# Kernel optimization log

Hardware: AMD Instinct MI355X
Metric: run time of the kernel (lower is better)

The kernel has to match this reference:

```python
import jax, jax.numpy as jnp
import numpy as np

HIDDEN = 1024
N_HEAD = 16
HEAD_DIM = HIDDEN // N_HEAD


def setup_inputs() -> dict:
    key = jax.random.key(0)
    k1, k2, k3 = jax.random.split(key, 3)
    B, S = 4, 2048
    x = jax.random.normal(k1, (B, S, HIDDEN), dtype=jnp.float32)
    # nn.Linear(hidden, 3*hidden, bias=False): weight [3*hidden, hidden]
    w_qkv = jax.random.normal(k2, (3 * HIDDEN, HIDDEN), dtype=jnp.float32) * (HIDDEN ** -0.5)
    w_out = jax.random.normal(k3, (HIDDEN, HIDDEN), dtype=jnp.float32) * (HIDDEN ** -0.5)
    return {"x": x, "w_qkv": w_qkv, "w_out": w_out}


def _rope(q, k):
    # q, k: [B, H, S, D]
    S, D = q.shape[-2], q.shape[-1]
    pos = jnp.arange(S, dtype=jnp.float32)[:, None]          # [S, 1]
    ids = jnp.arange(D // 2, dtype=jnp.float32)              # [D/2]
    theta = jnp.power(jnp.float32(10000.0), 2.0 * ids / D)   # [D/2]
    ang = pos / theta                                        # [S, D/2]
    # torch code: sin at even slots, cos at odd slots; then repeat_interleave(2)
    sin = jnp.repeat(jnp.sin(ang), 2, axis=-1)               # [S, D]
    cos = jnp.repeat(jnp.cos(ang), 2, axis=-1)               # [S, D]

    def rot(t):
        # stack([-t_odd, t_even], -1).reshape -> interleaved rotate-half
        t2 = jnp.stack([-t[..., 1::2], t[..., 0::2]], axis=-1).reshape(t.shape)
        return t * cos + t2 * sin

    return rot(q), rot(k)


def reference(x, w_qkv, w_out):
    B, S, _ = x.shape
    qkv = jnp.einsum('bsd,ed->bse', x, w_qkv)                # [B, S, 3*hidden]
    qkv = qkv.reshape(B, S, N_HEAD, 3 * HEAD_DIM).transpose(0, 2, 1, 3)  # [B,H,S,3D]
    q, k, v = jnp.split(qkv, 3, axis=-1)                     # each [B,H,S,D]
    q, k = _rope(q, k)
    # NOTE: original forward never applies self.scale, mask (eval), or dropout.
    scores = jnp.einsum('bhqd,bhkd->bhqk', q, k)             # [B,H,S,S]
    probs = jax.nn.softmax(scores, axis=-1)
    out = jnp.einsum('bhqk,bhkd->bhqd', probs, v)            # [B,H,S,D]
    out = out.transpose(0, 2, 1, 3).reshape(B, S, HIDDEN)
    return jnp.einsum('bsd,ed->bse', out, w_out)
```

## Files before the change

kernel.cpp:

```cpp
#include <hip/hip_runtime.h>
#include <stdint.h>
#include <math.h>

#define NHEAD 16
#define HDIM 64
#define BATCH 4
#define SEQ 2048
#define NROWS (BATCH*SEQ)
#define LOG2E 1.4426950408889634f

typedef _Float16 f16x8 __attribute__((ext_vector_type(8)));
typedef _Float16 f16x4 __attribute__((ext_vector_type(4)));
typedef __fp16 h16x2 __attribute__((ext_vector_type(2)));
typedef float f32x4 __attribute__((ext_vector_type(4)));
typedef float f32x16 __attribute__((ext_vector_type(16)));
typedef unsigned int u32x4 __attribute__((ext_vector_type(4)));

typedef const __attribute__((address_space(1))) unsigned int* gas_ptr;
typedef __attribute__((address_space(3))) unsigned int* las_ptr;

__device__ __forceinline__ void gload_lds16(const void* g, void* l) {
  __builtin_amdgcn_global_load_lds((gas_ptr)g, (las_ptr)l, 16, 0, 0);
}

__device__ __forceinline__ float exp2_fast(float x) {
  float r; asm("v_exp_f32 %0, %1" : "=v"(r) : "v"(x)); return r;
}

__device__ __forceinline__ unsigned pku(float a, float b) {
  h16x2 p = __builtin_amdgcn_cvt_pkrtz(a, b);
  return __builtin_bit_cast(unsigned, p);
}

__global__ void cvt_f16_kernel(const float* __restrict__ in,
                               unsigned short* __restrict__ out, int n4) {
  int stride = gridDim.x * blockDim.x;
  for (int i = blockIdx.x * blockDim.x + threadIdx.x; i < n4; i += stride) {
    float4 v = ((const float4*)in)[i];
    f16x4 h;
    h[0] = (_Float16)v.x; h[1] = (_Float16)v.y;
    h[2] = (_Float16)v.z; h[3] = (_Float16)v.w;
    ((f16x4*)out)[i] = h;
  }
}

__global__ void sincos_kernel(float2* __restrict__ tab) {
  int idx = blockIdx.x * blockDim.x + threadIdx.x;
  int s = idx >> 5, i = idx & 31;
  float theta = powf(10000.0f, (float)i / 32.0f);
  float ang = (float)s / theta;
  tab[idx] = make_float2(sinf(ang), cosf(ang));
}

__global__ __launch_bounds__(256)
void gemm_qkv_f16(const unsigned short* __restrict__ A,
                  const unsigned short* __restrict__ B,
                  const float2* __restrict__ tab,
                  unsigned short* __restrict__ Qh,
                  unsigned short* __restrict__ Kh,
                  unsigned short* __restrict__ Vt) {
  const int K = 1024, N = 3072, nk = K >> 5;
  __shared__ unsigned short sA[2][128 * 32];
  __shared__ unsigned short sB[2][128 * 32];
  const int tid = threadIdx.x;
  const int lane = tid & 63;
  const int wave = tid >> 6;
  const int wr = wave >> 1, wc = wave & 1;
  const long m0 = (long)blockIdx.x * 128;
  const long n0 = (long)blockIdx.y * 128;

  f32x4 acc[4][4] = {};

  const int o0 = tid * 16;
  const int row0_ = o0 >> 6;
  const int colb0 = o0 & 63;

  auto stage = [&](int buf, int kt) {
    const long k0 = (long)kt * 32;
    const char* Ab = (const char*)A;
    const char* Bb = (const char*)B;
    gload_lds16(Ab + ((m0 + row0_) * K + k0) * 2 + colb0,      (char*)&sA[buf][0] + o0);
    gload_lds16(Ab + ((m0 + row0_ + 64) * K + k0) * 2 + colb0, (char*)&sA[buf][0] + o0 + 4096);
    gload_lds16(Bb + ((n0 + row0_) * K + k0) * 2 + colb0,      (char*)&sB[buf][0] + o0);
    gload_lds16(Bb + ((n0 + row0_ + 64) * K + k0) * 2 + colb0, (char*)&sB[buf][0] + o0 + 4096);
  };

  stage(0, 0);
  __syncthreads();
  int cur = 0;
  const int kq = (lane >> 4) * 8;
  const int rA = wr * 64 + (lane & 15);
  const int rB = wc * 64 + (lane & 15);

  for (int kt = 0; kt < nk; ++kt) {
    if (kt + 1 < nk) stage(cur ^ 1, kt + 1);
    f16x8 af[4], bfr[4];
#pragma unroll
    for (int m = 0; m < 4; ++m)
      af[m] = *(const f16x8*)&sA[cur][(rA + m * 16) * 32 + kq];
#pragma unroll
    for (int n = 0; n < 4; ++n)
      bfr[n] = *(const f16x8*)&sB[cur][(rB + n * 16) * 32 + kq];
#pragma unroll
    for (int m = 0; m < 4; ++m)
#pragma unroll
      for (int n = 0; n < 4; ++n)
        acc[m][n] = __builtin_amdgcn_mfma_f32_16x16x32_f16(af[m], bfr[n], acc[m][n], 0, 0, 0);
    __syncthreads();
    cur ^= 1;
  }

  const int lhi = lane >> 4, llo = lane & 15;
  const long rbase = m0 + wr * 64 + (lhi << 2);
  const long cbase = n0 + wc * 64 + llo;
#pragma unroll
  for (int m = 0; m < 4; ++m)
#pragma unroll
    for (int n = 0; n < 4; ++n)
#pragma unroll
      for (int r = 0; r < 4; ++r) {
        int row = (int)(rbase + m * 16 + r);
        int col = (int)(cbase + n * 16);
        float v = acc[m][n][r];
        float p = __shfl_xor(v, 1, 64);
        int s = row & 2047, b = row >> 11;
        int h = col / 192, off = col % 192;
        int part = off >> 6, d = off & 63;
        long bh_ = b * 16 + h;
        if (part < 2) {
          float2 sc = tab[s * 32 + (d >> 1)];
          float rot = (d & 1) ? (v * sc.y + p * sc.x) : (v * sc.y - p * sc.x);
          long idx = (bh_ * SEQ + s) * 64 + d;
          if (part == 0) ((_Float16*)Qh)[idx] = (_Float16)(rot * LOG2E);
          else           ((_Float16*)Kh)[idx] = (_Float16)rot;
        } else {
          ((_Float16*)Vt)[(bh_ * 64 + d) * SEQ + s] = (_Float16)v;
        }
      }
}

__global__ __launch_bounds__(512, 3)
void attn_kernel(const unsigned short* __restrict__ Qh,
                 const unsigned short* __restrict__ Kh,
                 const unsigned short* __restrict__ Vt,
                 unsigned short* __restrict__ AOut) {
  __shared__ unsigned short sK[2][64 * 64];
  __shared__ unsigned short sV[2][64 * 64];

  const int tid = threadIdx.x;
  const int w = tid >> 6, lane = tid & 63;
  const int q32 = lane & 31, hi = lane >> 5;
  const int bh = blockIdx.y, b = bh >> 4, h = bh & 15;
  const int q = blockIdx.x * 256 + w * 32 + q32;

  f16x8 aq[4];
#pragma unroll
  for (int ds = 0; ds < 4; ++ds)
    aq[ds] = *(const f16x8*)&Qh[((long)bh * SEQ + q) * 64 + ds * 16 + hi * 8];

  f32x16 acc0 = {}, acc1 = {};
  float mrow = -INFINITY, lrow = 0.f;

  const int r7 = q32 & 7;
  int off[2][4];
#pragma unroll
  for (int t = 0; t < 2; ++t)
#pragma unroll
    for (int s = 0; s < 4; ++s)
      off[t][s] = (t * 32 + q32) * 64 + (((s * 2 + hi) ^ r7) << 3);

  const int cr = tid >> 3, cp = tid & 7, cps = cp ^ (cr & 7);
  const long kSrc0 = ((long)bh * SEQ + cr) * 64 + cps * 8;
  const long vSrc0 = ((long)bh * 64 + cr) * SEQ + cps * 8;

  auto stage = [&](int buf, int kt) {
    gload_lds16(&Kh[kSrc0 + (long)kt * 4096], (char*)&sK[buf][0] + tid * 16);
    gload_lds16(&Vt[vSrc0 + (long)kt * 64],   (char*)&sV[buf][0] + tid * 16);
  };

  stage(0, 0);
  __syncthreads();

#define MKPA(dst, S, R0) {                                        \
    unsigned A0 = pku(S[R0 + 0], S[R0 + 1]);                      \
    unsigned A1 = pku(S[R0 + 2], S[R0 + 3]);                      \
    unsigned B0 = pku(S[R0 + 4], S[R0 + 5]);                      \
    unsigned B1 = pku(S[R0 + 6], S[R0 + 7]);                      \
    asm("v_permlane32_swap_b32 %0, %1" : "+v"(A0), "+v"(B0));     \
    asm("v_permlane32_swap_b32 %0, %1" : "+v"(A1), "+v"(B1));     \
    u32x4 tt; tt[0] = A0; tt[1] = A1; tt[2] = B0; tt[3] = B1;     \
    dst = __builtin_bit_cast(f16x8, tt); }

#pragma unroll 2
  for (int kt = 0; kt < SEQ / 64; ++kt) {
    const int cur = kt & 1;
    if (kt + 1 < SEQ / 64) stage(cur ^ 1, kt + 1);
    const unsigned short* Kb = &sK[cur][0];
    const unsigned short* Vb = &sV[cur][0];

    f32x16 s0v = {}, s1v = {};
    __builtin_amdgcn_s_setprio(1);
#pragma unroll
    for (int ds = 0; ds < 4; ++ds) {
      f16x8 k0 = *(const f16x8*)&Kb[off[0][ds]];
      f16x8 k1 = *(const f16x8*)&Kb[off[1][ds]];
      s0v = __builtin_amdgcn_mfma_f32_32x32x16_f16(k0, aq[ds], s0v, 0, 0, 0);
      s1v = __builtin_amdgcn_mfma_f32_32x32x16_f16(k1, aq[ds], s1v, 0, 0, 0);
    }
    __builtin_amdgcn_s_setprio(0);

    float ta[16];
#pragma unroll
    for (int r = 0; r < 16; ++r) ta[r] = fmaxf(s0v[r], s1v[r]);
#pragma unroll
    for (int d = 8; d > 0; d >>= 1)
#pragma unroll
      for (int r = 0; r < d; ++r) ta[r] = fmaxf(ta[r], ta[r + d]);
    float tmax = fmaxf(ta[0], __shfl_xor(ta[0], 32, 64));

    if (__any(tmax > mrow + 8.0f)) {
      float mnew = fmaxf(mrow, tmax);
      float al = exp2_fast(mrow - mnew);
      mrow = mnew;
#pragma unroll
      for (int r = 0; r < 16; ++r) { acc0[r] *= al; acc1[r] *= al; }
      lrow *= al;
    }
    const float mr = mrow;

#pragma unroll
    for (int r = 0; r < 16; ++r) {
      s0v[r] = exp2_fast(s0v[r] - mr);
      s1v[r] = exp2_fast(s1v[r] - mr);
    }

    float sa[16];
#pragma unroll
    for (int r = 0; r < 16; ++r) sa[r] = s0v[r] + s1v[r];
#pragma unroll
    for (int d = 8; d > 0; d >>= 1)
#pragma unroll
      for (int r = 0; r < d; ++r) sa[r] = sa[r] + sa[r + d];
    lrow += sa[0] + __shfl_xor(sa[0], 32, 64);

    f16x8 pa[4];
    MKPA(pa[0], s0v, 0);
    MKPA(pa[1], s0v, 8);
    MKPA(pa[2], s1v, 0);
    MKPA(pa[3], s1v, 8);

    __builtin_amdgcn_s_setprio(1);
#pragma unroll
    for (int ks = 0; ks < 4; ++ks) {
      f16x8 v0 = *(const f16x8*)&Vb[off[0][ks]];
      f16x8 v1 = *(const f16x8*)&Vb[off[1][ks]];
      acc0 = __builtin_amdgcn_mfma_f32_32x32x16_f16(v0, pa[ks], acc0, 0, 0, 0);
      acc1 = __builtin_amdgcn_mfma_f32_32x32x16_f16(v1, pa[ks], acc1, 0, 0, 0);
    }
    __builtin_amdgcn_s_setprio(0);
    __syncthreads();
  }

  float inv = 1.f / lrow;
  const long obase = ((long)b * SEQ + q) * 1024 + h * 64;
#define EPI(ACCV, DT)                                              \
  {                                                                \
    _Pragma("unroll")                                              \
    for (int rg = 0; rg < 4; ++rg) {                               \
      f16x4 o;                                                     \
      _Pragma("unroll")                                            \
      for (int e = 0; e < 4; ++e)                                  \
        o[e] = (_Float16)(ACCV[rg * 4 + e] * inv);                 \
      *(f16x4*)&AOut[obase + DT * 32 + rg * 8 + hi * 4] = o;       \
    }                                                              \
  }
  EPI(acc0, 0);
  EPI(acc1, 1);
}

__global__ __launch_bounds__(256)
void gemm_out_f16(const unsigned short* __restrict__ A,
                  const unsigned short* __restrict__ B,
                  float* __restrict__ C, int M, int N, int K) {
  __shared__ unsigned short sA[2][128 * 32];
  __shared__ unsigned short sB[2][128 * 32];
  const int tid = threadIdx.x;
  const int lane = tid & 63;
  const int wave = tid >> 6;
  const int wr = wave >> 1, wc = wave & 1;
  const long m0 = (long)blockIdx.x * 128;
  const long n0 = (long)blockIdx.y * 128;

  f32x4 acc[4][4] = {};

  const int o0 = tid * 16;
  const int row0_ = o0 >> 6;
  const int colb0 = o0 & 63;

  auto stage = [&](int buf, int kt) {
    const long k0 = (long)kt * 32;
    const char* Ab = (const char*)A;
    const char* Bb = (const char*)B;
    gload_lds16(Ab + ((m0 + row0_) * K + k0) * 2 + colb0,      (char*)&sA[buf][0] + o0);
    gload_lds16(Ab + ((m0 + row0_ + 64) * K + k0) * 2 + colb0, (char*)&sA[buf][0] + o0 + 4096);
    gload_lds16(Bb + ((n0 + row0_) * K + k0) * 2 + colb0,      (char*)&sB[buf][0] + o0);
    gload_lds16(Bb + ((n0 + row0_ + 64) * K + k0) * 2 + colb0, (char*)&sB[buf][0] + o0 + 4096);
  };

  const int nk = K >> 5;
  stage(0, 0);
  __syncthreads();
  int cur = 0;
  const int kq = (lane >> 4) * 8;
  const int rA = wr * 64 + (lane & 15);
  const int rB = wc * 64 + (lane & 15);

  for (int kt = 0; kt < nk; ++kt) {
    if (kt + 1 < nk) stage(cur ^ 1, kt + 1);
    f16x8 af[4], bfr[4];
#pragma unroll
    for (int m = 0; m < 4; ++m)
      af[m] = *(const f16x8*)&sA[cur][(rA + m * 16) * 32 + kq];
#pragma unroll
    for (int n = 0; n < 4; ++n)
      bfr[n] = *(const f16x8*)&sB[cur][(rB + n * 16) * 32 + kq];
#pragma unroll
    for (int m = 0; m < 4; ++m)
#pragma unroll
      for (int n = 0; n < 4; ++n)
        acc[m][n] = __builtin_amdgcn_mfma_f32_16x16x32_f16(af[m], bfr[n], acc[m][n], 0, 0, 0);
    __syncthreads();
    cur ^= 1;
  }

  const long rbase = m0 + wr * 64 + ((lane >> 4) << 2);
  const long cbase = n0 + wc * 64 + (lane & 15);
#pragma unroll
  for (int m = 0; m < 4; ++m)
#pragma unroll
    for (int n = 0; n < 4; ++n)
#pragma unroll
      for (int r = 0; r < 4; ++r) {
        long row = rbase + m * 16 + r;
        long col = cbase + n * 16;
        C[row * N + col] = acc[m][n][r];
      }
}

extern "C" void kernel_launch(void* const* d_in, const int* in_sizes, int n_in,
                              void* d_out, int out_size, void* d_ws, size_t ws_size,
                              hipStream_t stream) {
  const float* x     = (const float*)d_in[0];
  const float* w_qkv = (const float*)d_in[1];
  const float* w_out = (const float*)d_in[2];
  float* out = (float*)d_out;
  char* ws = (char*)d_ws;

  unsigned short* xb    = (unsigned short*)(ws + 0);
  unsigned short* attnb = xb;
  unsigned short* wqkvb = (unsigned short*)(ws + 16777216);
  unsigned short* woutb = (unsigned short*)(ws + 23068672);
  unsigned short* Qh    = (unsigned short*)(ws + 25165824);
  unsigned short* Kh    = (unsigned short*)(ws + 41943040);
  unsigned short* Vt    = (unsigned short*)(ws + 58720256);
  float2*         tab   = (float2*)(ws + 75497472);

  cvt_f16_kernel<<<2048, 256, 0, stream>>>(x, xb, NROWS * 1024 / 4);
  cvt_f16_kernel<<<1024, 256, 0, stream>>>(w_qkv, wqkvb, 3072 * 1024 / 4);
  cvt_f16_kernel<<<512, 256, 0, stream>>>(w_out, woutb, 1024 * 1024 / 4);
  sincos_kernel<<<SEQ * 32 / 256, 256, 0, stream>>>(tab);

  gemm_qkv_f16<<<dim3(64, 24), 256, 0, stream>>>(xb, wqkvb, tab, Qh, Kh, Vt);
  attn_kernel<<<dim3(SEQ / 256, 64), 512, 0, stream>>>(Qh, Kh, Vt, attnb);
  gemm_out_f16<<<dim3(64, 8), 256, 0, stream>>>(attnb, woutb, out, NROWS, 1024, 1024);
}
```

Before: 241.6 us.

## Double K-tile depth to 64 with XOR-swizzled LDS in both GEMMs

Both the QKV and output GEMMs now stage 64-wide K tiles instead of 32, which halves the number of barrier iterations and issues two MFMAs per fragment pair. The LDS layout uses an XOR swizzle on 16-byte chunks to avoid bank conflicts on the wider rows. The QKV epilogue is restructured to hoist the head/part decoding per column out of the inner loops. The cost is twice the LDS use per block, which may lower occupancy.

```diff
diff --git a/kernel.cpp b/kernel.cpp
--- a/kernel.cpp
+++ b/kernel.cpp
@@ -59,9 +59,9 @@
                   unsigned short* __restrict__ Qh,
                   unsigned short* __restrict__ Kh,
                   unsigned short* __restrict__ Vt) {
-  const int K = 1024, N = 3072, nk = K >> 5;
-  __shared__ unsigned short sA[2][128 * 32];
-  __shared__ unsigned short sB[2][128 * 32];
+  const int K = 1024, nk = K >> 6;
+  __shared__ unsigned short sA[2][128 * 64];
+  __shared__ unsigned short sB[2][128 * 64];
   const int tid = threadIdx.x;
   const int lane = tid & 63;
   const int wave = tid >> 6;
@@ -71,72 +71,91 @@
 
   f32x4 acc[4][4] = {};
 
-  const int o0 = tid * 16;
-  const int row0_ = o0 >> 6;
-  const int colb0 = o0 & 63;
-
   auto stage = [&](int buf, int kt) {
-    const long k0 = (long)kt * 32;
+    const long k0 = (long)kt * 64;
     const char* Ab = (const char*)A;
     const char* Bb = (const char*)B;
-    gload_lds16(Ab + ((m0 + row0_) * K + k0) * 2 + colb0,      (char*)&sA[buf][0] + o0);
-    gload_lds16(Ab + ((m0 + row0_ + 64) * K + k0) * 2 + colb0, (char*)&sA[buf][0] + o0 + 4096);
-    gload_lds16(Bb + ((n0 + row0_) * K + k0) * 2 + colb0,      (char*)&sB[buf][0] + o0);
-    gload_lds16(Bb + ((n0 + row0_ + 64) * K + k0) * 2 + colb0, (char*)&sB[buf][0] + o0 + 4096);
+#pragma unroll
+    for (int qd = 0; qd < 4; ++qd) {
+      int o = qd * 4096 + tid * 16;
+      int row = o >> 7;
+      int colb = (((o >> 4) & 7) ^ (row & 7)) << 4;
+      gload_lds16(Ab + ((m0 + row) * K + k0) * 2 + colb, (char*)&sA[buf][0] + o);
+      gload_lds16(Bb + ((n0 + row) * K + k0) * 2 + colb, (char*)&sB[buf][0] + o);
+    }
   };
+
+  const int lhi = lane >> 4, llo = lane & 15;
+  const int rA = wr * 64 + llo;
+  const int rB = wc * 64 + llo;
+  int chsw[2];
+#pragma unroll
+  for (int s = 0; s < 2; ++s) chsw[s] = (((s * 4 + lhi) ^ (llo & 7)) << 3);
 
   stage(0, 0);
   __syncthreads();
   int cur = 0;
-  const int kq = (lane >> 4) * 8;
-  const int rA = wr * 64 + (lane & 15);
-  const int rB = wc * 64 + (lane & 15);
 
   for (int kt = 0; kt < nk; ++kt) {
     if (kt + 1 < nk) stage(cur ^ 1, kt + 1);
-    f16x8 af[4], bfr[4];
+    f16x8 af[2][4], bfr[2][4];
+#pragma unroll
+    for (int s = 0; s < 2; ++s)
+#pragma unroll
+      for (int m = 0; m < 4; ++m)
+        af[s][m] = *(const f16x8*)&sA[cur][(rA + m * 16) * 64 + chsw[s]];
+#pragma unroll
+    for (int s = 0; s < 2; ++s)
+#pragma unroll
+      for (int n = 0; n < 4; ++n)
+        bfr[s][n] = *(const f16x8*)&sB[cur][(rB + n * 16) * 64 + chsw[s]];
 #pragma unroll
     for (int m = 0; m < 4; ++m)
-      af[m] = *(const f16x8*)&sA[cur][(rA + m * 16) * 32 + kq];
-#pragma unroll
-    for (int n = 0; n < 4; ++n)
-      bfr[n] = *(const f16x8*)&sB[cur][(rB + n * 16) * 32 + kq];
-#pragma unroll
-    for (int m = 0; m < 4; ++m)
-#pragma unroll
-      for (int n = 0; n < 4; ++n)
-        acc[m][n] = __builtin_amdgcn_mfma_f32_16x16x32_f16(af[m], bfr[n], acc[m][n], 0, 0, 0);
+#pragma unroll
+      for (int n = 0; n < 4; ++n) {
+        acc[m][n] = __builtin_amdgcn_mfma_f32_16x16x32_f16(af[0][m], bfr[0][n], acc[m][n], 0, 0, 0);
+        acc[m][n] = __builtin_amdgcn_mfma_f32_16x16x32_f16(af[1][m], bfr[1][n], acc[m][n], 0, 0, 0);
+      }
     __syncthreads();
     cur ^= 1;
   }
 
-  const int lhi = lane >> 4, llo = lane & 15;
-  const long rbase = m0 + wr * 64 + (lhi << 2);
-  const long cbase = n0 + wc * 64 + llo;
-#pragma unroll
-  for (int m = 0; m < 4; ++m)
-#pragma unroll
-    for (int n = 0; n < 4; ++n)
-#pragma unroll
-      for (int r = 0; r < 4; ++r) {
-        int row = (int)(rbase + m * 16 + r);
-        int col = (int)(cbase + n * 16);
-        float v = acc[m][n][r];
-        float p = __shfl_xor(v, 1, 64);
-        int s = row & 2047, b = row >> 11;
-        int h = col / 192, off = col % 192;
-        int part = off >> 6, d = off & 63;
-        long bh_ = b * 16 + h;
-        if (part < 2) {
-          float2 sc = tab[s * 32 + (d >> 1)];
-          float rot = (d & 1) ? (v * sc.y + p * sc.x) : (v * sc.y - p * sc.x);
-          long idx = (bh_ * SEQ + s) * 64 + d;
-          if (part == 0) ((_Float16*)Qh)[idx] = (_Float16)(rot * LOG2E);
-          else           ((_Float16*)Kh)[idx] = (_Float16)rot;
-        } else {
-          ((_Float16*)Vt)[(bh_ * 64 + d) * SEQ + s] = (_Float16)v;
+  const int rb0 = (int)m0 + wr * 64 + lhi * 4;
+  const int bidx = rb0 >> 11;
+  const int s0 = rb0 & 2047;
+#pragma unroll
+  for (int n = 0; n < 4; ++n) {
+    const int col = (int)n0 + wc * 64 + llo + n * 16;
+    const int h = col / 192;
+    const int off = col - h * 192;
+    const int part = off >> 6;
+    const int d = off & 63;
+    const long bh_ = (long)(bidx * 16 + h);
+    if (part < 2) {
+      _Float16* dst = (_Float16*)(part == 0 ? Qh : Kh) + bh_ * SEQ * 64 + d;
+      const float qs = (part == 0) ? LOG2E : 1.0f;
+      const float2* tp = tab + (d >> 1);
+      const int sgn = d & 1;
+#pragma unroll
+      for (int m = 0; m < 4; ++m)
+#pragma unroll
+        for (int r = 0; r < 4; ++r) {
+          int s = s0 + m * 16 + r;
+          float v = acc[m][n][r];
+          float p = __shfl_xor(v, 1, 64);
+          float2 sc = tp[s * 32];
+          float rot = sgn ? (v * sc.y + p * sc.x) : (v * sc.y - p * sc.x);
+          dst[(long)s * 64] = (_Float16)(rot * qs);
         }
-      }
+    } else {
+      _Float16* dst = (_Float16*)Vt + (bh_ * 64 + d) * SEQ;
+#pragma unroll
+      for (int m = 0; m < 4; ++m)
+#pragma unroll
+        for (int r = 0; r < 4; ++r)
+          dst[s0 + m * 16 + r] = (_Float16)acc[m][n][r];
+    }
+  }
 }
 
 __global__ __launch_bounds__(512, 3)
@@ -282,8 +301,8 @@
 void gemm_out_f16(const unsigned short* __restrict__ A,
                   const unsigned short* __restrict__ B,
                   float* __restrict__ C, int M, int N, int K) {
-  __shared__ unsigned short sA[2][128 * 32];
-  __shared__ unsigned short sB[2][128 * 32];
+  __shared__ unsigned short sA[2][128 * 64];
+  __shared__ unsigned short sB[2][128 * 64];
   const int tid = threadIdx.x;
   const int lane = tid & 63;
   const int wave = tid >> 6;
@@ -293,58 +312,66 @@
 
   f32x4 acc[4][4] = {};
 
-  const int o0 = tid * 16;
-  const int row0_ = o0 >> 6;
-  const int colb0 = o0 & 63;
-
   auto stage = [&](int buf, int kt) {
-    const long k0 = (long)kt * 32;
+    const long k0 = (long)kt * 64;
     const char* Ab = (const char*)A;
     const char* Bb = (const char*)B;
-    gload_lds16(Ab + ((m0 + row0_) * K + k0) * 2 + colb0,      (char*)&sA[buf][0] + o0);
-    gload_lds16(Ab + ((m0 + row0_ + 64) * K + k0) * 2 + colb0, (char*)&sA[buf][0] + o0 + 4096);
-    gload_lds16(Bb + ((n0 + row0_) * K + k0) * 2 + colb0,      (char*)&sB[buf][0] + o0);
-    gload_lds16(Bb + ((n0 + row0_ + 64) * K + k0) * 2 + colb0, (char*)&sB[buf][0] + o0 + 4096);
+#pragma unroll
+    for (int qd = 0; qd < 4; ++qd) {
+      int o = qd * 4096 + tid * 16;
+      int row = o >> 7;
+      int colb = (((o >> 4) & 7) ^ (row & 7)) << 4;
+      gload_lds16(Ab + ((m0 + row) * K + k0) * 2 + colb, (char*)&sA[buf][0] + o);
+      gload_lds16(Bb + ((n0 + row) * K + k0) * 2 + colb, (char*)&sB[buf][0] + o);
+    }
   };
 
-  const int nk = K >> 5;
+  const int lhi = lane >> 4, llo = lane & 15;
+  const int rA = wr * 64 + llo;
+  const int rB = wc * 64 + llo;
+  int chsw[2];
+#pragma unroll
+  for (int s = 0; s < 2; ++s) chsw[s] = (((s * 4 + lhi) ^ (llo & 7)) << 3);
+
+  const int nk = K >> 6;
   stage(0, 0);
   __syncthreads();
   int cur = 0;
-  const int kq = (lane >> 4) * 8;
-  const int rA = wr * 64 + (lane & 15);
-  const int rB = wc * 64 + (lane & 15);
 
   for (int kt = 0; kt < nk; ++kt) {
     if (kt + 1 < nk) stage(cur ^ 1, kt + 1);
-    f16x8 af[4], bfr[4];
+    f16x8 af[2][4], bfr[2][4];
+#pragma unroll
+    for (int s = 0; s < 2; ++s)
+#pragma unroll
+      for (int m = 0; m < 4; ++m)
+        af[s][m] = *(const f16x8*)&sA[cur][(rA + m * 16) * 64 + chsw[s]];
+#pragma unroll
+    for (int s = 0; s < 2; ++s)
+#pragma unroll
+      for (int n = 0; n < 4; ++n)
+        bfr[s][n] = *(const f16x8*)&sB[cur][(rB + n * 16) * 64 + chsw[s]];
 #pragma unroll
     for (int m = 0; m < 4; ++m)
-      af[m] = *(const f16x8*)&sA[cur][(rA + m * 16) * 32 + kq];
-#pragma unroll
-    for (int n = 0; n < 4; ++n)
-      bfr[n] = *(const f16x8*)&sB[cur][(rB + n * 16) * 32 + kq];
-#pragma unroll
-    for (int m = 0; m < 4; ++m)
-#pragma unroll
-      for (int n = 0; n < 4; ++n)
-        acc[m][n] = __builtin_amdgcn_mfma_f32_16x16x32_f16(af[m], bfr[n], acc[m][n], 0, 0, 0);
+#pragma unroll
+      for (int n = 0; n < 4; ++n) {
+        acc[m][n] = __builtin_amdgcn_mfma_f32_16x16x32_f16(af[0][m], bfr[0][n], acc[m][n], 0, 0, 0);
+        acc[m][n] = __builtin_amdgcn_mfma_f32_16x16x32_f16(af[1][m], bfr[1][n], acc[m][n], 0, 0, 0);
+      }
     __syncthreads();
     cur ^= 1;
   }
 
-  const long rbase = m0 + wr * 64 + ((lane >> 4) << 2);
-  const long cbase = n0 + wc * 64 + (lane & 15);
-#pragma unroll
-  for (int m = 0; m < 4; ++m)
-#pragma unroll
-    for (int n = 0; n < 4; ++n)
-#pragma unroll
-      for (int r = 0; r < 4; ++r) {
-        long row = rbase + m * 16 + r;
-        long col = cbase + n * 16;
-        C[row * N + col] = acc[m][n][r];
-      }
+  const long rbase = m0 + wr * 64 + lhi * 4;
+#pragma unroll
+  for (int n = 0; n < 4; ++n) {
+    const long col = n0 + wc * 64 + llo + n * 16;
+#pragma unroll
+    for (int m = 0; m < 4; ++m)
+#pragma unroll
+      for (int r = 0; r < 4; ++r)
+        C[(rbase + m * 16 + r) * N + col] = acc[m][n][r];
+  }
 }
 
 extern "C" void kernel_launch(void* const* d_in, const int* in_sizes, int n_in,
```

Result: faster. 213.1 us (-11.8%).
